# Performance work log

Hardware: AMD Instinct MI355X
Metric: run time of the kernel (lower is better)

## Reference

```python
import jax, jax.numpy as jnp
import numpy as np

B, T, V, E, H, C = 64, 512, 100000, 300, 128, 20  # H = hidden//2 per direction


def setup_inputs() -> dict:
    key = jax.random.key(0)
    ks = jax.random.split(key, 16)
    s = 0.05
    x = jax.random.randint(ks[0], (B, T), 0, V)
    lengths = jax.random.randint(ks[1], (B,), T // 4, T + 1)
    mask = jnp.arange(T)[None, :] < lengths[:, None]           # [B,T] bool
    tags = jax.random.randint(ks[2], (B, T), 0, C)
    emb = (jax.random.normal(ks[3], (V, E)) * s).at[0].set(0.0)  # padding_idx=0 zeroed
    W_ih_f = jax.random.normal(ks[4], (4 * H, E)) * s
    W_hh_f = jax.random.normal(ks[5], (4 * H, H)) * s
    b_ih_f = jax.random.normal(ks[6], (4 * H,)) * s
    b_hh_f = jax.random.normal(ks[7], (4 * H,)) * s
    W_ih_b = jax.random.normal(ks[8], (4 * H, E)) * s
    W_hh_b = jax.random.normal(ks[9], (4 * H, H)) * s
    b_ih_b = jax.random.normal(ks[10], (4 * H,)) * s
    b_hh_b = jax.random.normal(ks[11], (4 * H,)) * s
    fc_W = jax.random.normal(ks[12], (C, 2 * H)) * s
    fc_b = jax.random.normal(ks[13], (C,)) * s
    transitions = jax.random.uniform(ks[14], (C, C), minval=-0.1, maxval=0.1)
    return dict(x=x, mask=mask, tags=tags, emb=emb,
                W_ih_f=W_ih_f, W_hh_f=W_hh_f, b_ih_f=b_ih_f, b_hh_f=b_hh_f,
                W_ih_b=W_ih_b, W_hh_b=W_hh_b, b_ih_b=b_ih_b, b_hh_b=b_hh_b,
                fc_W=fc_W, fc_b=fc_b, transitions=transitions)


def _lstm_dir(xe, W_ih, W_hh, b_ih, b_hh):
    # xe: [B,T,E]; torch LSTM gate order i,f,g,o
    b, t, _ = xe.shape
    h_dim = W_hh.shape[1]
    xw = jnp.einsum('bte,ge->btg', xe, W_ih) + b_ih + b_hh      # [B,T,4H]

    def step(carry, xw_t):
        h, c = carry
        g = xw_t + h @ W_hh.T
        i, f, gg, o = jnp.split(g, 4, axis=-1)
        i = jax.nn.sigmoid(i); f = jax.nn.sigmoid(f)
        gg = jnp.tanh(gg); o = jax.nn.sigmoid(o)
        c = f * c + i * gg
        h = o * jnp.tanh(c)
        return (h, c), h

    init = (jnp.zeros((b, h_dim), xe.dtype), jnp.zeros((b, h_dim), xe.dtype))
    _, hs = jax.lax.scan(step, init, jnp.swapaxes(xw, 0, 1))    # [T,B,H]
    return jnp.swapaxes(hs, 0, 1)


def _crf_nll(logits, tags, mask, transitions):
    maskf = mask.astype(logits.dtype)
    # log partition (forward algorithm)
    em_t = jnp.swapaxes(logits, 0, 1)                           # [T,B,C]
    m_t = jnp.swapaxes(mask, 0, 1)                              # [T,B]

    def part_step(log_alpha, inp):
        emit_t, mt = inp
        scores = log_alpha[:, :, None] + transitions[None] + emit_t[:, None, :]
        la = jax.nn.logsumexp(scores, axis=1)
        return jnp.where(mt[:, None], la, log_alpha), None

    log_alpha, _ = jax.lax.scan(part_step, em_t[0], (em_t[1:], m_t[1:]))
    log_den = jax.nn.logsumexp(log_alpha, axis=1)               # [B]
    # joint log likelihood of gold path
    emit_score = jnp.take_along_axis(logits, tags[..., None], axis=2)[..., 0]
    pair = transitions[tags[:, :-1], tags[:, 1:]]               # [B,T-1]
    pm = (mask[:, 1:] & mask[:, :-1]).astype(logits.dtype)
    log_num = (emit_score * maskf).sum(axis=1) + (pair * pm).sum(axis=1)
    return jnp.mean(log_den - log_num)


def reference(x, mask, tags, emb, W_ih_f, W_hh_f, b_ih_f, b_hh_f,
              W_ih_b, W_hh_b, b_ih_b, b_hh_b, fc_W, fc_b, transitions):
    xe = emb[x]                                                 # [B,T,E]
    h_f = _lstm_dir(xe, W_ih_f, W_hh_f, b_ih_f, b_hh_f)
    h_b = _lstm_dir(xe[:, ::-1], W_ih_b, W_hh_b, b_ih_b, b_hh_b)[:, ::-1]
    out = jnp.concatenate([h_f, h_b], axis=-1)                  # [B,T,2H]
    logits = out @ fc_W.T + fc_b                                # [B,T,C]
    loss = _crf_nll(logits, tags, mask, transitions)
    return loss, logits
```

## Files before the change

### kernel.cpp

```cpp
#include <hip/hip_runtime.h>
#include <hip/hip_bf16.h>
#include <hip/hip_fp16.h>

typedef unsigned short u16;
typedef unsigned char u8;
typedef unsigned int u32;
typedef __attribute__((ext_vector_type(8))) short short8;
typedef __attribute__((ext_vector_type(4))) float f32x4;
typedef __attribute__((ext_vector_type(2))) _Float16 half2_t;

#define B_ 64
#define T_ 512
#define E_ 300
#define KP_ 320
#define H_ 128
#define G_ 512
#define C_ 20
#define NCH_ 32
#define CS_ 16

__device__ __forceinline__ float b2f(u16 u) {
    union { u32 i; float f; } v; v.i = ((u32)u) << 16; return v.f;
}
__device__ __forceinline__ u16 f2b(float f) {
    union { float f; u32 i; } v; v.f = f;
    u32 r = (v.i + 0x7fffu + ((v.i >> 16) & 1u)) >> 16;
    return (u16)r;
}
__device__ __forceinline__ float loadf(const void* p, long i, u32 isf32) {
    return isf32 ? ((const float*)p)[i] : b2f(((const u16*)p)[i]);
}
__device__ __forceinline__ float sigmoidf_(float x) {
    return 1.0f / (1.0f + __expf(-x));
}
__device__ __forceinline__ float tanhf_(float x) {
    float cx = fminf(fmaxf(x, -15.f), 15.f);
    float e = __expf(2.f * cx);
    return (e - 1.f) / (e + 1.f);
}
__device__ __forceinline__ int loadmask(const void* m, int idx, u32 isbool) {
    return isbool ? (int)((const u8*)m)[idx] : ((const int*)m)[idx];
}
__device__ __forceinline__ u16 f2h(float f) {
    __half h = __float2half(f);
    return __half_as_ushort(h);
}
__device__ __forceinline__ float dot2f(u32 a, u32 b, float c) {
#if __has_builtin(__builtin_amdgcn_fdot2)
    return __builtin_amdgcn_fdot2(__builtin_bit_cast(half2_t, a),
                                  __builtin_bit_cast(half2_t, b), c, false);
#else
    half2_t av = __builtin_bit_cast(half2_t, a);
    half2_t bv = __builtin_bit_cast(half2_t, b);
    return c + (float)av.x * (float)bv.x + (float)av.y * (float)bv.y;
#endif
}

__global__ void sniff_kernel(const u32* __restrict__ emb32,
                             const u32* __restrict__ mask32,
                             u32* __restrict__ flags) {
    if (threadIdx.x == 0) {
        u32 nz = 0;
        for (int i = 150; i < 300; ++i) nz |= emb32[i];
        flags[0] = (nz == 0) ? 1u : 0u;
        u32 m0 = mask32[0];
        flags[1] = ((m0 & 0xFFFFFF00u) != 0) ? 1u : 0u;
    }
}

__global__ __launch_bounds__(256) void prep_kernel(
    const void* __restrict__ Wihf, const void* __restrict__ Wihb,
    const void* __restrict__ Whhf, const void* __restrict__ Whhb,
    const void* __restrict__ bihf, const void* __restrict__ bhhf,
    const void* __restrict__ bihb, const void* __restrict__ bhhb,
    const void* __restrict__ fcW, const void* __restrict__ fcb,
    const void* __restrict__ trans, const u32* __restrict__ flags,
    u16* __restrict__ Wpad, u32* __restrict__ Whh2, float* __restrict__ biasc,
    u16* __restrict__ fcWc, float* __restrict__ fcbf, float* __restrict__ transf) {
    const u32 isf32 = flags[0];
    int idx = blockIdx.x * 256 + threadIdx.x;
    if (idx < 2 * G_ * KP_) {
        int dir = idx / (G_ * KP_), rem = idx % (G_ * KP_);
        int g = rem / KP_, kp = rem % KP_;
        const void* src = dir ? Wihb : Wihf;
        float v = (kp < E_) ? loadf(src, (long)g * E_ + kp, isf32) : 0.f;
        Wpad[idx] = f2b(v);
        return;
    }
    idx -= 2 * G_ * KP_;
    if (idx < 2 * G_ * 64) {
        int dir = idx >> 15, rem = idx & 32767;
        int row = rem >> 6, k2 = rem & 63;
        const void* src = dir ? Whhb : Whhf;
        float w0 = loadf(src, (long)row * H_ + 2 * k2, isf32);
        float w1 = loadf(src, (long)row * H_ + 2 * k2 + 1, isf32);
        Whh2[idx] = (u32)f2h(w0) | ((u32)f2h(w1) << 16);
        return;
    }
    idx -= 2 * G_ * 64;
    if (idx < 2 * G_) {
        int dir = idx >> 9, g = idx & 511;
        biasc[idx] = loadf(dir ? bihb : bihf, g, isf32) +
                     loadf(dir ? bhhb : bhhf, g, isf32);
        return;
    }
    idx -= 2 * G_;
    if (idx < C_ * 256) { fcWc[idx] = f2b(loadf(fcW, idx, isf32)); return; }
    idx -= C_ * 256;
    if (idx < C_) { fcbf[idx] = loadf(fcb, idx, isf32); return; }
    idx -= C_;
    if (idx < C_ * C_) { transf[idx] = loadf(trans, idx, isf32); return; }
}

__global__ __launch_bounds__(256) void gemm_xw(const int* __restrict__ x,
                                               const void* __restrict__ emb,
                                               const u16* __restrict__ Wpad,
                                               const float* __restrict__ biasc,
                                               const u32* __restrict__ flags,
                                               u16* __restrict__ xwf, u16* __restrict__ xwb,
                                               int tclog2, int t0f, int t0b) {
    const int m0 = blockIdx.x * 128;
    const int n0 = blockIdx.y * 128;
    const int dir = blockIdx.z;
    const u16* Bw = Wpad + (size_t)dir * G_ * KP_;
    u16* out = dir ? xwb : xwf;
    const int t0 = dir ? t0b : t0f;
    const int ts = dir ? -1 : 1;
    const int tcm = (1 << tclog2) - 1;
    const u32 isf32 = flags[0];

    __shared__ __align__(16) short As[128 * 32];
    __shared__ __align__(16) short Bs[128 * 32];
    __shared__ int xs[128];

    const int tid = threadIdx.x;
    const int lane = tid & 63;
    const int wave = tid >> 6;
    const int wm = wave & 1, wn = wave >> 1;
    const int lr = lane & 15, lq = lane >> 4;

    if (tid < 128) {
        int i = m0 + tid;
        int b = i >> tclog2;
        int r = i & tcm;
        xs[tid] = x[b * T_ + t0 + ts * r];
    }
    __syncthreads();

    f32x4 acc[4][4];
#pragma unroll
    for (int mt = 0; mt < 4; ++mt)
#pragma unroll
        for (int nt = 0; nt < 4; ++nt)
            acc[mt][nt] = (f32x4){0.f, 0.f, 0.f, 0.f};

    for (int kb = 0; kb < KP_; kb += 32) {
        if (isf32) {
            const float* ef = (const float*)emb;
#pragma unroll
            for (int hh = 0; hh < 4; ++hh) {
                int c = tid + hh * 256;
                int row = c >> 3;
                int k4 = (c & 7) * 4;
                int k = kb + k4;
                uint2 o = make_uint2(0u, 0u);
                if (k < E_) {
                    float4 v = *(const float4*)(ef + (size_t)xs[row] * E_ + k);
                    o.x = (u32)f2b(v.x) | ((u32)f2b(v.y) << 16);
                    o.y = (u32)f2b(v.z) | ((u32)f2b(v.w) << 16);
                }
                *(uint2*)(&As[row * 32 + k4]) = o;
            }
        } else {
            const u16* eb = (const u16*)emb;
#pragma unroll
            for (int hh = 0; hh < 4; ++hh) {
                int c = tid + hh * 256;
                int row = c >> 3;
                int k4 = (c & 7) * 4;
                int k = kb + k4;
                uint2 va = make_uint2(0u, 0u);
                if (k < E_)
                    va = *(const uint2*)(eb + (size_t)xs[row] * E_ + k);
                *(uint2*)(&As[row * 32 + k4]) = va;
            }
        }
#pragma unroll
        for (int hh = 0; hh < 2; ++hh) {
            int c = tid + hh * 256;
            int row = c >> 2;
            int k8 = (c & 3) * 8;
            uint4 vb = *(const uint4*)(Bw + (size_t)(n0 + row) * KP_ + kb + k8);
            *(uint4*)(&Bs[row * 32 + k8]) = vb;
        }
        __syncthreads();
        short8 afr[4], bfr[4];
#pragma unroll
        for (int mt = 0; mt < 4; ++mt)
            afr[mt] = *(const short8*)&As[(wm * 64 + mt * 16 + lr) * 32 + lq * 8];
#pragma unroll
        for (int nt = 0; nt < 4; ++nt)
            bfr[nt] = *(const short8*)&Bs[(wn * 64 + nt * 16 + lr) * 32 + lq * 8];
#pragma unroll
        for (int mt = 0; mt < 4; ++mt)
#pragma unroll
            for (int nt = 0; nt < 4; ++nt)
                acc[mt][nt] = __builtin_amdgcn_mfma_f32_16x16x32_bf16(afr[mt], bfr[nt], acc[mt][nt], 0, 0, 0);
        __syncthreads();
    }
#pragma unroll
    for (int nt = 0; nt < 4; ++nt) {
        int n = n0 + wn * 64 + nt * 16 + lr;
        float bn = biasc[dir * G_ + n];
#pragma unroll
        for (int mt = 0; mt < 4; ++mt) {
            int mbase = m0 + wm * 64 + mt * 16 + lq * 4;
#pragma unroll
            for (int r = 0; r < 4; ++r)
                out[(size_t)(mbase + r) * G_ + n] = f2b(acc[mt][nt][r] + bn);
        }
    }
}

#define DOTQ(wq, hq) \
    acc = dot2f(wq.x, hq.x, acc); acc = dot2f(wq.y, hq.y, acc); \
    acc = dot2f(wq.z, hq.z, acc); acc = dot2f(wq.w, hq.w, acc);

__global__ __launch_bounds__(512, 1) void lstm_kernel(const u32* __restrict__ Whh2,
                                                      const u16* __restrict__ xwf,
                                                      const u16* __restrict__ xwb,
                                                      u16* __restrict__ hf,
                                                      u16* __restrict__ hb,
                                                      float* __restrict__ carry,
                                                      int TC, int t0f, int t0b, int first) {
    const int b = blockIdx.x;
    const int dir = blockIdx.y;
    const int tid = threadIdx.x;
    const int j = tid >> 2;
    const int gq = tid & 3;
    const int row = gq * H_ + j;
    const u16* xw = (dir ? xwb : xwf) + (size_t)b * TC * G_ + row;
    u16* hout = (dir ? hb : hf) + (size_t)b * T_ * H_;
    const int t0 = dir ? t0b : t0f;
    const int ts = dir ? -1 : 1;
    float* carry_c = carry + (size_t)(dir * B_ + b) * H_;
    float* carry_h = carry + (size_t)(2 * B_ + dir * B_ + b) * H_;

    const uint4* W4 = (const uint4*)(Whh2 + (size_t)dir * G_ * 64 + (size_t)row * 64);
    uint4 w0 = W4[0],  w1 = W4[1],  w2 = W4[2],  w3 = W4[3];
    uint4 w4 = W4[4],  w5 = W4[5],  w6 = W4[6],  w7 = W4[7];
    uint4 w8 = W4[8],  w9 = W4[9],  w10 = W4[10], w11 = W4[11];
    uint4 w12 = W4[12], w13 = W4[13], w14 = W4[14], w15 = W4[15];

    __shared__ __align__(16) u32 hs2[2][64];

    float c0 = first ? 0.f : carry_c[j];
    if (tid < 64) {
        float ha = first ? 0.f : carry_h[2 * tid];
        float hb2 = first ? 0.f : carry_h[2 * tid + 1];
        hs2[0][tid] = (u32)f2h(ha) | ((u32)f2h(hb2) << 16);
    }
    __syncthreads();

    const int lane = tid & 63;
    const int lbase = lane & ~3;
    int cur = 0;
    float xv = b2f(xw[0]);
    float hlast = 0.f;
    for (int r = 0; r < TC; ++r) {
        float xv_n = 0.f;
        if (r + 1 < TC) xv_n = b2f(xw[(size_t)(r + 1) * G_]);
        const uint4* hp = (const uint4*)hs2[cur];
        float acc = 0.f;
        { uint4 hq = hp[0];  DOTQ(w0, hq) }
        { uint4 hq = hp[1];  DOTQ(w1, hq) }
        { uint4 hq = hp[2];  DOTQ(w2, hq) }
        { uint4 hq = hp[3];  DOTQ(w3, hq) }
        { uint4 hq = hp[4];  DOTQ(w4, hq) }
        { uint4 hq = hp[5];  DOTQ(w5, hq) }
        { uint4 hq = hp[6];  DOTQ(w6, hq) }
        { uint4 hq = hp[7];  DOTQ(w7, hq) }
        { uint4 hq = hp[8];  DOTQ(w8, hq) }
        { uint4 hq = hp[9];  DOTQ(w9, hq) }
        { uint4 hq = hp[10]; DOTQ(w10, hq) }
        { uint4 hq = hp[11]; DOTQ(w11, hq) }
        { uint4 hq = hp[12]; DOTQ(w12, hq) }
        { uint4 hq = hp[13]; DOTQ(w13, hq) }
        { uint4 hq = hp[14]; DOTQ(w14, hq) }
        { uint4 hq = hp[15]; DOTQ(w15, hq) }
        float g = xv + acc;
        float v = (gq == 2) ? tanhf_(g) : sigmoidf_(g);
        float vi = __shfl(v, lbase + 0, 64);
        float vf = __shfl(v, lbase + 1, 64);
        float vg = __shfl(v, lbase + 2, 64);
        float vo = __shfl(v, lbase + 3, 64);
        c0 = vf * c0 + vi * vg;
        float h = vo * tanhf_(c0);
        hlast = h;
        float hnxt = __shfl(h, lane + 4, 64);
        if (gq == 0) {
            hout[(size_t)(t0 + ts * r) * H_ + j] = f2b(h);
            if ((j & 1) == 0)
                hs2[cur ^ 1][j >> 1] = (u32)f2h(h) | ((u32)f2h(hnxt) << 16);
        }
        __syncthreads();
        cur ^= 1;
        xv = xv_n;
    }
    if (gq == 0) { carry_c[j] = c0; carry_h[j] = hlast; }
}

__global__ __launch_bounds__(256) void fc_kernel(const u16* __restrict__ hf,
                                                 const u16* __restrict__ hb,
                                                 const u16* __restrict__ fcWc,
                                                 const float* __restrict__ fcbf,
                                                 const u32* __restrict__ flags,
                                                 float* __restrict__ logits,
                                                 void* __restrict__ dout) {
    __shared__ float Ws[C_ * 256];
    __shared__ float Hs[16 * 256];
    const int tid = threadIdx.x;
    const int bt0 = blockIdx.x * 64;
    const u32 isf32 = flags[0];
#pragma unroll
    for (int i = 0; i < C_; ++i) {
        int v = tid + i * 256;
        Ws[v] = b2f(fcWc[v]);
    }
    __syncthreads();
    for (int grp = 0; grp < 4; ++grp) {
        int btg = bt0 + grp * 16;
#pragma unroll
        for (int i = 0; i < 16; ++i) {
            int v = tid + i * 256;
            int r = v >> 8, k = v & 255;
            Hs[v] = (k < H_) ? b2f(hf[(size_t)(btg + r) * H_ + k])
                             : b2f(hb[(size_t)(btg + r) * H_ + (k - H_)]);
        }
        __syncthreads();
#pragma unroll
        for (int q = 0; q < 2; ++q) {
            int p = tid + q * 256;
            if (p < 16 * C_) {
                int r = p / C_, cc = p % C_;
                float acc = fcbf[cc];
                const float* wr = &Ws[cc * 256];
                const float* hr = &Hs[r * 256];
#pragma unroll
                for (int k = 0; k < 256; k += 4)
                    acc += wr[k] * hr[k] + wr[k + 1] * hr[k + 1] +
                           wr[k + 2] * hr[k + 2] + wr[k + 3] * hr[k + 3];
                size_t o = (size_t)(btg + r) * C_ + cc;
                logits[o] = acc;
                if (isf32) ((float*)dout)[1 + o] = acc;
                else       ((u16*)dout)[1 + o] = f2b(acc);
            }
        }
        __syncthreads();
    }
}

__global__ __launch_bounds__(512) void crf_chunk(const float* __restrict__ logits,
                                                 const void* __restrict__ mask,
                                                 const float* __restrict__ transf,
                                                 const u32* __restrict__ flags,
                                                 float* __restrict__ Mc) {
    const int c = blockIdx.x;
    const int b = blockIdx.y;
    const int p = threadIdx.x;
    const bool act = p < C_ * C_;
    const int i = p / C_, j = p % C_;
    const u32 isbool = flags[1];

    __shared__ float P[C_ * C_];
    float trj[C_];
    if (act) {
#pragma unroll
        for (int k = 0; k < C_; ++k) trj[k] = transf[k * C_ + j];
        P[p] = (i == j) ? 0.f : -1e30f;
    }
    __syncthreads();

    const float* lg = logits + (size_t)b * T_ * C_;
    const int t0 = 1 + CS_ * c;

    float e = 0.f; int mk = 0;
    if (act) e = lg[(size_t)t0 * C_ + j];
    mk = loadmask(mask, b * T_ + t0, isbool);

    for (int s = 0; s < CS_; ++s) {
        int t = t0 + s;
        if (t >= T_) break;
        float e_n = 0.f; int mk_n = 0;
        int tn = t + 1;
        if (s + 1 < CS_ && tn < T_) {
            if (act) e_n = lg[(size_t)tn * C_ + j];
            mk_n = loadmask(mask, b * T_ + tn, isbool);
        }
        float nv = 0.f;
        if (act) {
            float sv[C_];
            float mx = -3e38f;
#pragma unroll
            for (int k = 0; k < C_; ++k) {
                sv[k] = P[i * C_ + k] + trj[k];
                mx = fmaxf(mx, sv[k]);
            }
            float sum = 0.f;
#pragma unroll
            for (int k = 0; k < C_; ++k) sum += __expf(sv[k] - mx);
            float la = mx + __logf(sum) + e;
            nv = mk ? la : P[p];
        }
        __syncthreads();
        if (act) P[p] = nv;
        __syncthreads();
        e = e_n; mk = mk_n;
    }
    if (act) Mc[((size_t)b * NCH_ + c) * (C_ * C_) + p] = P[p];
}

__global__ __launch_bounds__(64) void crf_combine(const float* __restrict__ logits,
                                                  const float* __restrict__ Mc,
                                                  float* __restrict__ log_den) {
    const int b = blockIdx.x;
    const int j = threadIdx.x;
    const bool act = j < C_;
    __shared__ float alpha[C_];
    const float* lg = logits + (size_t)b * T_ * C_;
    const float* mb = Mc + (size_t)b * NCH_ * (C_ * C_);
    if (act) alpha[j] = lg[j];
    __syncthreads();

    float mc[C_], mcn[C_];
    if (act) {
#pragma unroll
        for (int i = 0; i < C_; ++i) mc[i] = mb[i * C_ + j];
    }
    for (int c = 0; c < NCH_; ++c) {
        if (act && c + 1 < NCH_) {
#pragma unroll
            for (int i = 0; i < C_; ++i) mcn[i] = mb[(size_t)(c + 1) * (C_ * C_) + i * C_ + j];
        }
        float nv = 0.f;
        if (act) {
            float sv[C_];
            float mx = -3e38f;
#pragma unroll
            for (int i = 0; i < C_; ++i) {
                sv[i] = alpha[i] + mc[i];
                mx = fmaxf(mx, sv[i]);
            }
            float sum = 0.f;
#pragma unroll
            for (int i = 0; i < C_; ++i) sum += __expf(sv[i] - mx);
            nv = mx + __logf(sum);
        }
        __syncthreads();
        if (act) alpha[j] = nv;
        __syncthreads();
#pragma unroll
        for (int i = 0; i < C_; ++i) mc[i] = mcn[i];
    }
    if (j == 0) {
        float mx = -3e38f;
#pragma unroll
        for (int i = 0; i < C_; ++i) mx = fmaxf(mx, alpha[i]);
        float sum = 0.f;
#pragma unroll
        for (int i = 0; i < C_; ++i) sum += __expf(alpha[i] - mx);
        log_den[b] = mx + __logf(sum);
    }
}

__global__ __launch_bounds__(64) void loss_partial(const float* __restrict__ logits,
                                                   const void* __restrict__ mask,
                                                   const int* __restrict__ tags,
                                                   const float* __restrict__ transf,
                                                   const u32* __restrict__ flags,
                                                   float* __restrict__ num) {
    const int b = blockIdx.x;
    const int lane = threadIdx.x;
    const u32 isbool = flags[1];
    const float* lg = logits + (size_t)b * T_ * C_;
    const int* tg = tags + b * T_;
    float s = 0.f;
    for (int t = lane; t < T_; t += 64) {
        int tt = tg[t];
        int mm = loadmask(mask, b * T_ + t, isbool);
        if (mm) s += lg[(size_t)t * C_ + tt];
        if (t >= 1) {
            int tp = tg[t - 1];
            int mp = loadmask(mask, b * T_ + t - 1, isbool);
            if (mm && mp) s += transf[tp * C_ + tt];
        }
    }
#pragma unroll
    for (int off = 32; off >= 1; off >>= 1)
        s += __shfl_down(s, off, 64);
    if (lane == 0) num[b] = s;
}

__global__ __launch_bounds__(64) void loss_final(const float* __restrict__ den,
                                                 const float* __restrict__ num,
                                                 const u32* __restrict__ flags,
                                                 void* __restrict__ dout) {
    const int b = threadIdx.x;
    float v = den[b] - num[b];
#pragma unroll
    for (int off = 32; off >= 1; off >>= 1)
        v += __shfl_down(v, off, 64);
    if (b == 0) {
        float loss = v * (1.0f / B_);
        if (flags[0]) ((float*)dout)[0] = loss;
        else          ((u16*)dout)[0] = f2b(loss);
    }
}

extern "C" void kernel_launch(void* const* d_in, const int* in_sizes, int n_in,
                              void* d_out, int out_size, void* d_ws, size_t ws_size,
                              hipStream_t stream) {
    const int* x     = (const int*)d_in[0];
    const void* mask = d_in[1];
    const int* tags  = (const int*)d_in[2];
    const void* emb  = d_in[3];
    const void* Wihf = d_in[4];
    const void* Whhf = d_in[5];
    const void* bihf = d_in[6];
    const void* bhhf = d_in[7];
    const void* Wihb = d_in[8];
    const void* Whhb = d_in[9];
    const void* bihb = d_in[10];
    const void* bhhb = d_in[11];
    const void* fcW  = d_in[12];
    const void* fcb  = d_in[13];
    const void* trans= d_in[14];

    char* ws = (char*)d_ws;
    u32*   flags = (u32*)(ws + 0);
    u16*   Wpad  = (u16*)(ws + 256);
    u32*   Whh2  = (u32*)(ws + 655616);
    float* biasc = (float*)(ws + 917760);
    u16*   fcWc  = (u16*)(ws + 921856);
    float* fcbf  = (float*)(ws + 932096);
    float* transf= (float*)(ws + 932224);
    u16*   hf    = (u16*)(ws + 933888);
    u16*   hb    = (u16*)(ws + 9322496);
    float* lgf   = (float*)(ws + 17711104);
    float* den   = (float*)(ws + 20332544);
    float* carry = (float*)(ws + 20332800);
    float* Mc    = (float*)(ws + 20463872);
    float* numb  = (float*)(ws + 23740672);
    const size_t xw_off = 23740928;

    int TC, lg2;
    if (ws_size >= xw_off + 2ull * 65536ull * 512ull + 4096ull)      { TC = 512; lg2 = 9; }
    else if (ws_size >= xw_off + 2ull * 65536ull * 256ull + 4096ull) { TC = 256; lg2 = 8; }
    else if (ws_size >= xw_off + 2ull * 65536ull * 128ull + 4096ull) { TC = 128; lg2 = 7; }
    else if (ws_size >= xw_off + 2ull * 65536ull * 64ull + 4096ull)  { TC = 64;  lg2 = 6; }
    else                                                             { TC = 32;  lg2 = 5; }
    u16* xwf = (u16*)(ws + xw_off);
    u16* xwb = (u16*)(ws + xw_off + (size_t)65536 * TC);

    hipLaunchKernelGGL(sniff_kernel, dim3(1), dim3(64), 0, stream,
                       (const u32*)emb, (const u32*)mask, flags);
    hipLaunchKernelGGL(prep_kernel, dim3(1562), dim3(256), 0, stream,
                       Wihf, Wihb, Whhf, Whhb, bihf, bhhf, bihb, bhhb,
                       fcW, fcb, trans, flags, Wpad, Whh2, biasc, fcWc, fcbf, transf);

    const int nc = T_ / TC;
    for (int ci = 0; ci < nc; ++ci) {
        int t0f = ci * TC;
        int t0b = T_ - 1 - ci * TC;
        hipLaunchKernelGGL(gemm_xw, dim3((B_ * TC) / 128, 4, 2), dim3(256), 0, stream,
                           x, emb, Wpad, biasc, flags, xwf, xwb, lg2, t0f, t0b);
        hipLaunchKernelGGL(lstm_kernel, dim3(B_, 2), dim3(512), 0, stream,
                           Whh2, xwf, xwb, hf, hb, carry, TC, t0f, t0b, (ci == 0) ? 1 : 0);
    }

    hipLaunchKernelGGL(fc_kernel, dim3(512), dim3(256), 0, stream,
                       hf, hb, fcWc, fcbf, flags, lgf, d_out);
    hipLaunchKernelGGL(crf_chunk, dim3(NCH_, B_), dim3(512), 0, stream,
                       lgf, mask, transf, flags, Mc);
    hipLaunchKernelGGL(crf_combine, dim3(B_), dim3(64), 0, stream, lgf, Mc, den);
    hipLaunchKernelGGL(loss_partial, dim3(B_), dim3(64), 0, stream,
                       lgf, mask, tags, transf, flags, numb);
    hipLaunchKernelGGL(loss_final, dim3(1), dim3(64), 0, stream, den, numb, flags, d_out);
}
```

Before: 880.1 us.

## Compute all four LSTM gates per thread with 128-thread blocks

Restructures the recurrent LSTM kernel so each of 128 threads owns one hidden unit and computes all four gate dot products itself. The previous design used 512 threads with cross-lane shuffles to combine gates. The xw GEMM output is permuted so a thread's four gate preactivations sit together and load as a single uint2. Each thread keeps 256 VGPRs of recurrent weights (loaded via inline asm), and xw loads are prefetched two steps ahead. This removes the shuffles and shrinks the per-step barrier to two waves, at the cost of 4x serial FMA work per thread and very high register pressure.

New measurement: 1.070 ms. 21.6% more time.

```diff
diff --git a/kernel.cpp b/kernel.cpp
--- a/kernel.cpp
+++ b/kernel.cpp
@@ -212,102 +212,108 @@
     for (int nt = 0; nt < 4; ++nt) {
         int n = n0 + wn * 64 + nt * 16 + lr;
         float bn = biasc[dir * G_ + n];
+        int np = ((n & 127) << 2) | (n >> 7);
 #pragma unroll
         for (int mt = 0; mt < 4; ++mt) {
             int mbase = m0 + wm * 64 + mt * 16 + lq * 4;
 #pragma unroll
             for (int r = 0; r < 4; ++r)
-                out[(size_t)(mbase + r) * G_ + n] = f2b(acc[mt][nt][r] + bn);
-        }
-    }
-}
-
-#define DOTQ(wq, hq) \
+                out[(size_t)(mbase + r) * G_ + np] = f2b(acc[mt][nt][r] + bn);
+        }
+    }
+}
+
+#define DOTQ4(acc, wq, hq) \
     acc = dot2f(wq.x, hq.x, acc); acc = dot2f(wq.y, hq.y, acc); \
     acc = dot2f(wq.z, hq.z, acc); acc = dot2f(wq.w, hq.w, acc);
 
-__global__ __launch_bounds__(512, 1) void lstm_kernel(const u32* __restrict__ Whh2,
-                                                      const u16* __restrict__ xwf,
-                                                      const u16* __restrict__ xwb,
-                                                      u16* __restrict__ hf,
-                                                      u16* __restrict__ hb,
-                                                      float* __restrict__ carry,
-                                                      int TC, int t0f, int t0b, int first) {
+#define GLD(dst, ptr, OFF) \
+    asm volatile("global_load_dwordx4 %0, %1, off offset:" OFF : "=v"(dst) : "v"(ptr))
+
+#define STEP_I(n) { uint4 hq = hp[n]; \
+    DOTQ4(aI, wi##n, hq) DOTQ4(aF, wf##n, hq) \
+    DOTQ4(aG, wg##n, hq) DOTQ4(aO, wo##n, hq) }
+
+__global__ __launch_bounds__(128)
+__attribute__((amdgpu_waves_per_eu(1, 1)))
+void lstm_kernel(const u32* __restrict__ Whh2,
+                 const u16* __restrict__ xwf,
+                 const u16* __restrict__ xwb,
+                 u16* __restrict__ hf,
+                 u16* __restrict__ hb,
+                 float* __restrict__ carry,
+                 int TC, int t0f, int t0b, int first) {
     const int b = blockIdx.x;
     const int dir = blockIdx.y;
-    const int tid = threadIdx.x;
-    const int j = tid >> 2;
-    const int gq = tid & 3;
-    const int row = gq * H_ + j;
-    const u16* xw = (dir ? xwb : xwf) + (size_t)b * TC * G_ + row;
+    const int j = threadIdx.x;
+    const u16* xw = (dir ? xwb : xwf) + (size_t)b * TC * G_ + 4 * j;
     u16* hout = (dir ? hb : hf) + (size_t)b * T_ * H_;
     const int t0 = dir ? t0b : t0f;
     const int ts = dir ? -1 : 1;
     float* carry_c = carry + (size_t)(dir * B_ + b) * H_;
     float* carry_h = carry + (size_t)(2 * B_ + dir * B_ + b) * H_;
 
-    const uint4* W4 = (const uint4*)(Whh2 + (size_t)dir * G_ * 64 + (size_t)row * 64);
-    uint4 w0 = W4[0],  w1 = W4[1],  w2 = W4[2],  w3 = W4[3];
-    uint4 w4 = W4[4],  w5 = W4[5],  w6 = W4[6],  w7 = W4[7];
-    uint4 w8 = W4[8],  w9 = W4[9],  w10 = W4[10], w11 = W4[11];
-    uint4 w12 = W4[12], w13 = W4[13], w14 = W4[14], w15 = W4[15];
-
-    __shared__ __align__(16) u32 hs2[2][64];
+    const u32* Wbase = Whh2 + (size_t)dir * G_ * 64;
+    const uint4* WI = (const uint4*)(Wbase + (size_t)(0 + j) * 64);
+    const uint4* WF = (const uint4*)(Wbase + (size_t)(128 + j) * 64);
+    const uint4* WG = (const uint4*)(Wbase + (size_t)(256 + j) * 64);
+    const uint4* WO = (const uint4*)(Wbase + (size_t)(384 + j) * 64);
+
+    uint4 wi0, wi1, wi2, wi3, wi4, wi5, wi6, wi7, wi8, wi9, wi10, wi11, wi12, wi13, wi14, wi15;
+    uint4 wf0, wf1, wf2, wf3, wf4, wf5, wf6, wf7, wf8, wf9, wf10, wf11, wf12, wf13, wf14, wf15;
+    uint4 wg0, wg1, wg2, wg3, wg4, wg5, wg6, wg7, wg8, wg9, wg10, wg11, wg12, wg13, wg14, wg15;
+    uint4 wo0, wo1, wo2, wo3, wo4, wo5, wo6, wo7, wo8, wo9, wo10, wo11, wo12, wo13, wo14, wo15;
+    GLD(wi0, WI, "0");    GLD(wi1, WI, "16");   GLD(wi2, WI, "32");   GLD(wi3, WI, "48");
+    GLD(wi4, WI, "64");   GLD(wi5, WI, "80");   GLD(wi6, WI, "96");   GLD(wi7, WI, "112");
+    GLD(wi8, WI, "128");  GLD(wi9, WI, "144");  GLD(wi10, WI, "160"); GLD(wi11, WI, "176");
+    GLD(wi12, WI, "192"); GLD(wi13, WI, "208"); GLD(wi14, WI, "224"); GLD(wi15, WI, "240");
+    GLD(wf0, WF, "0");    GLD(wf1, WF, "16");   GLD(wf2, WF, "32");   GLD(wf3, WF, "48");
+    GLD(wf4, WF, "64");   GLD(wf5, WF, "80");   GLD(wf6, WF, "96");   GLD(wf7, WF, "112");
+    GLD(wf8, WF, "128");  GLD(wf9, WF, "144");  GLD(wf10, WF, "160"); GLD(wf11, WF, "176");
+    GLD(wf12, WF, "192"); GLD(wf13, WF, "208"); GLD(wf14, WF, "224"); GLD(wf15, WF, "240");
+    GLD(wg0, WG, "0");    GLD(wg1, WG, "16");   GLD(wg2, WG, "32");   GLD(wg3, WG, "48");
+    GLD(wg4, WG, "64");   GLD(wg5, WG, "80");   GLD(wg6, WG, "96");   GLD(wg7, WG, "112");
+    GLD(wg8, WG, "128");  GLD(wg9, WG, "144");  GLD(wg10, WG, "160"); GLD(wg11, WG, "176");
+    GLD(wg12, WG, "192"); GLD(wg13, WG, "208"); GLD(wg14, WG, "224"); GLD(wg15, WG, "240");
+    GLD(wo0, WO, "0");    GLD(wo1, WO, "16");   GLD(wo2, WO, "32");   GLD(wo3, WO, "48");
+    GLD(wo4, WO, "64");   GLD(wo5, WO, "80");   GLD(wo6, WO, "96");   GLD(wo7, WO, "112");
+    GLD(wo8, WO, "128");  GLD(wo9, WO, "144");  GLD(wo10, WO, "160"); GLD(wo11, WO, "176");
+    GLD(wo12, WO, "192"); GLD(wo13, WO, "208"); GLD(wo14, WO, "224"); GLD(wo15, WO, "240");
+    asm volatile("s_waitcnt vmcnt(0)" ::: "memory");
+
+    __shared__ __align__(16) u16 hs2[2][H_];
 
     float c0 = first ? 0.f : carry_c[j];
-    if (tid < 64) {
-        float ha = first ? 0.f : carry_h[2 * tid];
-        float hb2 = first ? 0.f : carry_h[2 * tid + 1];
-        hs2[0][tid] = (u32)f2h(ha) | ((u32)f2h(hb2) << 16);
-    }
+    hs2[0][j] = first ? (u16)0 : f2h(carry_h[j]);
     __syncthreads();
 
-    const int lane = tid & 63;
-    const int lbase = lane & ~3;
     int cur = 0;
-    float xv = b2f(xw[0]);
+    uint2 xq  = *(const uint2*)(xw);
+    uint2 xq1 = (TC > 1) ? *(const uint2*)(xw + (size_t)1 * G_) : make_uint2(0u, 0u);
     float hlast = 0.f;
     for (int r = 0; r < TC; ++r) {
-        float xv_n = 0.f;
-        if (r + 1 < TC) xv_n = b2f(xw[(size_t)(r + 1) * G_]);
+        uint2 xq2 = make_uint2(0u, 0u);
+        if (r + 2 < TC) xq2 = *(const uint2*)(xw + (size_t)(r + 2) * G_);
         const uint4* hp = (const uint4*)hs2[cur];
-        float acc = 0.f;
-        { uint4 hq = hp[0];  DOTQ(w0, hq) }
-        { uint4 hq = hp[1];  DOTQ(w1, hq) }
-        { uint4 hq = hp[2];  DOTQ(w2, hq) }
-        { uint4 hq = hp[3];  DOTQ(w3, hq) }
-        { uint4 hq = hp[4];  DOTQ(w4, hq) }
-        { uint4 hq = hp[5];  DOTQ(w5, hq) }
-        { uint4 hq = hp[6];  DOTQ(w6, hq) }
-        { uint4 hq = hp[7];  DOTQ(w7, hq) }
-        { uint4 hq = hp[8];  DOTQ(w8, hq) }
-        { uint4 hq = hp[9];  DOTQ(w9, hq) }
-        { uint4 hq = hp[10]; DOTQ(w10, hq) }
-        { uint4 hq = hp[11]; DOTQ(w11, hq) }
-        { uint4 hq = hp[12]; DOTQ(w12, hq) }
-        { uint4 hq = hp[13]; DOTQ(w13, hq) }
-        { uint4 hq = hp[14]; DOTQ(w14, hq) }
-        { uint4 hq = hp[15]; DOTQ(w15, hq) }
-        float g = xv + acc;
-        float v = (gq == 2) ? tanhf_(g) : sigmoidf_(g);
-        float vi = __shfl(v, lbase + 0, 64);
-        float vf = __shfl(v, lbase + 1, 64);
-        float vg = __shfl(v, lbase + 2, 64);
-        float vo = __shfl(v, lbase + 3, 64);
-        c0 = vf * c0 + vi * vg;
-        float h = vo * tanhf_(c0);
+        float aI = 0.f, aF = 0.f, aG = 0.f, aO = 0.f;
+        STEP_I(0)  STEP_I(1)  STEP_I(2)  STEP_I(3)
+        STEP_I(4)  STEP_I(5)  STEP_I(6)  STEP_I(7)
+        STEP_I(8)  STEP_I(9)  STEP_I(10) STEP_I(11)
+        STEP_I(12) STEP_I(13) STEP_I(14) STEP_I(15)
+        float gi = sigmoidf_(b2f((u16)(xq.x & 0xffff)) + aI);
+        float gf = sigmoidf_(b2f((u16)(xq.x >> 16)) + aF);
+        float gg = tanhf_(b2f((u16)(xq.y & 0xffff)) + aG);
+        float go = sigmoidf_(b2f((u16)(xq.y >> 16)) + aO);
+        c0 = gf * c0 + gi * gg;
+        float h = go * tanhf_(c0);
         hlast = h;
-        float hnxt = __shfl(h, lane + 4, 64);
-        if (gq == 0) {
-            hout[(size_t)(t0 + ts * r) * H_ + j] = f2b(h);
-            if ((j & 1) == 0)
-                hs2[cur ^ 1][j >> 1] = (u32)f2h(h) | ((u32)f2h(hnxt) << 16);
-        }
+        hs2[cur ^ 1][j] = f2h(h);
+        hout[(size_t)(t0 + ts * r) * H_ + j] = f2b(h);
         __syncthreads();
         cur ^= 1;
-        xv = xv_n;
-    }
-    if (gq == 0) { carry_c[j] = c0; carry_h[j] = hlast; }
+        xq = xq1; xq1 = xq2;
+    }
+    carry_c[j] = c0; carry_h[j] = hlast;
 }
 
 __global__ __launch_bounds__(256) void fc_kernel(const u16* __restrict__ hf,
@@ -574,7 +580,7 @@
         int t0b = T_ - 1 - ci * TC;
         hipLaunchKernelGGL(gemm_xw, dim3((B_ * TC) / 128, 4, 2), dim3(256), 0, stream,
                            x, emb, Wpad, biasc, flags, xwf, xwb, lg2, t0f, t0b);
-        hipLaunchKernelGGL(lstm_kernel, dim3(B_, 2), dim3(512), 0, stream,
+        hipLaunchKernelGGL(lstm_kernel, dim3(B_, 2), dim3(128), 0, stream,
                            Whh2, xwf, xwb, hf, hb, carry, TC, t0f, t0b, (ci == 0) ? 1 : 0);
     }
 
```
